# Optimization experiments

Hardware: AMD Instinct MI355X
Metric: run time of the kernel (lower is better)

Reference implementation:

```python
import jax, jax.numpy as jnp
import numpy as np

N_TYPES = 4
D_DESC = 256
H = 256
N_ATOMS = 131072


def setup_inputs() -> dict:
    key = jax.random.key(0)
    ks = jax.random.split(key, 8)
    descriptors = jax.random.normal(ks[0], (N_ATOMS, D_DESC), dtype=jnp.float32)
    elems = jax.random.randint(ks[1], (N_ATOMS,), 0, N_TYPES, dtype=jnp.int32)
    # Per-type MLP params: stacked over the type axis T.
    s1 = 1.0 / np.sqrt(D_DESC)
    s2 = 1.0 / np.sqrt(H)
    W1 = jax.random.normal(ks[2], (N_TYPES, D_DESC, H), dtype=jnp.float32) * s1
    b1 = jnp.zeros((N_TYPES, H), dtype=jnp.float32)
    W2 = jax.random.normal(ks[3], (N_TYPES, H, H), dtype=jnp.float32) * s2
    b2 = jnp.zeros((N_TYPES, H), dtype=jnp.float32)
    W3 = jax.random.normal(ks[4], (N_TYPES, H), dtype=jnp.float32) * s2  # output dim 1, squeezed
    b3 = jnp.zeros((N_TYPES,), dtype=jnp.float32)
    return {"descriptors": descriptors, "elems": elems,
            "W1": W1, "b1": b1, "W2": W2, "b2": b2, "W3": W3, "b3": b3}


def reference(descriptors, elems, W1, b1, W2, b2, W3, b3):
    # Equivalent to: for each atom, run the MLP subnet of its element type and
    # scatter the scalar output back to the per-atom attribute vector.
    # Vectorized as batched-per-type GEMMs followed by a per-atom type gather
    # (dense dispatch: fixed shapes, jit-friendly).
    # h1: [T, N, H]
    h1 = jnp.tanh(jnp.einsum('nd,tdh->tnh', descriptors, W1) + b1[:, None, :])
    h2 = jnp.tanh(jnp.einsum('tnh,thk->tnk', h1, W2) + b2[:, None, :])
    out_t = jnp.einsum('tnh,th->tn', h2, W3) + b3[:, None]  # [T, N]
    # select per-atom row according to its element type
    per_atom = out_t[elems, jnp.arange(out_t.shape[1])]  # [N]
    return per_atom
```

## Files before the change

### kernel.cpp

```cpp
#include <hip/hip_runtime.h>
#include <stdint.h>


typedef __attribute__((ext_vector_type(8))) short short8;
typedef __attribute__((ext_vector_type(4))) float f32x4;

#define NPB 256
#define NTY 4

__device__ __forceinline__ unsigned short f2bf(float f) {
    union { float f; uint32_t u; } v; v.f = f;
    uint32_t u = v.u;
    uint32_t r = (u + 0x7FFFu + ((u >> 16) & 1u)) >> 16;
    return (unsigned short)r;
}
__device__ __forceinline__ float fast_tanh(float x) {
    x = fminf(fmaxf(x, -10.0f), 10.0f);
    float e = __expf(2.0f * x);
    return (e - 1.0f) * __builtin_amdgcn_rcpf(e + 1.0f);
}


__global__ void count_k(const int* __restrict__ elems, int n, int chunk,
                        int* __restrict__ counts) {
    __shared__ int h[NTY];
    if (threadIdx.x < NTY) h[threadIdx.x] = 0;
    __syncthreads();
    const int start = blockIdx.x * chunk;
    const int end   = min(start + chunk, n);
    for (int i = start + threadIdx.x; i < end; i += blockDim.x)
        atomicAdd(&h[elems[i]], 1);
    __syncthreads();
    if (threadIdx.x < NTY) counts[threadIdx.x * NPB + blockIdx.x] = h[threadIdx.x];
}

__global__ void prefix_k(const int* __restrict__ counts,
                         int* __restrict__ cursor, int* __restrict__ hdr) {
    __shared__ int tot[NTY];
    const int t = threadIdx.x;
    if (t < NTY) {
        int s = 0;
        for (int b = 0; b < NPB; ++b) s += counts[t * NPB + b];
        tot[t] = s;
    }
    __syncthreads();
    if (t == 0) {
        int b = 0, tb = 0;
        for (int ty = 0; ty < NTY; ++ty) {
            hdr[ty]      = tot[ty];
            hdr[8 + ty]  = b;
            hdr[12 + ty] = tb;
            b  += tot[ty];
            tb += (tot[ty] + 63) >> 6;
        }
        hdr[16] = tb;
    }
    __syncthreads();
    if (t < NTY) {
        int run = hdr[8 + t];
        for (int b = 0; b < NPB; ++b) {
            cursor[t * NPB + b] = run;
            run += counts[t * NPB + b];
        }
    }
}

__global__ void scatter_k(const int* __restrict__ elems, int n, int chunk,
                          const int* __restrict__ cursor, int* __restrict__ sorted) {
    __shared__ int cur[NTY];
    if (threadIdx.x < NTY) cur[threadIdx.x] = cursor[threadIdx.x * NPB + blockIdx.x];
    __syncthreads();
    const int start = blockIdx.x * chunk;
    const int end   = min(start + chunk, n);
    for (int i = start + threadIdx.x; i < end; i += blockDim.x) {
        int ty  = elems[i];
        int pos = atomicAdd(&cur[ty], 1);
        sorted[pos] = i;
    }
}

__global__ void wconv_k(const float* __restrict__ W1, const float* __restrict__ W2,
                        unsigned short* __restrict__ w1s, unsigned short* __restrict__ w2s) {
    int gid  = blockIdx.x * blockDim.x + threadIdx.x;
    int lane = gid & 63;
    int ks   = (gid >> 6) & 7;
    int tile = (gid >> 9) & 15;
    int t    = (gid >> 13) & 3;
    int layer = gid >> 15;
    const float* W = layer ? W2 : W1;
    unsigned short* o = layer ? w2s : w1s;
    int dbase = ks * 32 + ((lane >> 4) << 3);
    int col   = tile * 16 + (lane & 15);
    unsigned short v[8];
#pragma unroll
    for (int j = 0; j < 8; ++j)
        v[j] = f2bf(W[(size_t)t * 65536 + (size_t)(dbase + j) * 256 + col]);
    unsigned short* dst = o + ((size_t)(t * 16 + tile) * 8 + ks) * 512 + lane * 8;
    *(short8*)dst = *(short8*)v;
}

__global__ __launch_bounds__(256, 4) void mlp_k(
    const float* __restrict__ desc,
    const float* __restrict__ b1g,
    const float* __restrict__ b2g,
    const float* __restrict__ W3,
    const float* __restrict__ b3,
    const int* __restrict__ hdr,
    const int* __restrict__ sorted,
    const unsigned short* __restrict__ w1s,
    const unsigned short* __restrict__ w2s,
    float* __restrict__ out)
{
    __shared__ __align__(16) char buf[32768];
    __shared__ float biasLds[512];
    __shared__ float part[4][64];

    const int tid  = threadIdx.x;
    const int lane = tid & 63;
    const int w    = tid >> 6;

    const int total = hdr[16];
    const int b = blockIdx.x;
    if (b >= total) return;

    int t = 3;
    if      (b < hdr[13]) t = 0;
    else if (b < hdr[14]) t = 1;
    else if (b < hdr[15]) t = 2;
    const int tloc   = b - hdr[12 + t];
    const int cnt    = hdr[t];
    const int base   = hdr[8 + t];
    const int astart = tloc * 64;

    biasLds[tid]       = b1g[t * 256 + tid];
    biasLds[256 + tid] = b2g[t * 256 + tid];

    {
        const int slot = tid >> 2;
        const int q    = tid & 3;
        const int g    = astart + slot;
        const int idx  = (g < cnt) ? sorted[base + g] : -1;
        const float4* row = (const float4*)(desc + (size_t)(idx < 0 ? 0 : idx) * 256);
#pragma unroll
        for (int i = 0; i < 16; ++i) {
            const int f = q + i * 4;
            float4 v;
            if (idx >= 0) v = row[f];
            else          v = make_float4(0.f, 0.f, 0.f, 0.f);
            unsigned short h4[4];
            h4[0] = f2bf(v.x); h4[1] = f2bf(v.y);
            h4[2] = f2bf(v.z); h4[3] = f2bf(v.w);
            const int off = slot * 512 + ((f * 8) ^ ((slot & 7) << 4));
            *(ushort4*)(buf + off) = *(ushort4*)h4;
        }
    }
    __syncthreads();

    const unsigned short* w1t = w1s + (size_t)t * (16 * 8 * 512);
    const unsigned short* w2t = w2s + (size_t)t * (16 * 8 * 512);

    f32x4 acc[4][4];
#pragma unroll
    for (int q = 0; q < 4; ++q)
#pragma unroll
        for (int nt = 0; nt < 4; ++nt)
            acc[q][nt] = (f32x4){0.f, 0.f, 0.f, 0.f};

#pragma unroll
    for (int ks = 0; ks < 8; ++ks) {
        short8 af[4];
#pragma unroll
        for (int q = 0; q < 4; ++q)
            af[q] = *(const short8*)(w1t + ((size_t)((w * 4 + q) * 8 + ks)) * 512 + lane * 8);
        short8 bh[4];
        const int colb = ks * 64 + ((lane >> 4) << 4);
#pragma unroll
        for (int nt = 0; nt < 4; ++nt) {
            const int row = nt * 16 + (lane & 15);
            const int off = row * 512 + (colb ^ ((row & 7) << 4));
            bh[nt] = *(const short8*)(buf + off);
        }
#pragma unroll
        for (int q = 0; q < 4; ++q)
#pragma unroll
            for (int nt = 0; nt < 4; ++nt)
                acc[q][nt] = __builtin_amdgcn_mfma_f32_16x16x32_bf16(af[q], bh[nt], acc[q][nt], 0, 0, 0);
    }
    __syncthreads();

    {
#pragma unroll
        for (int q = 0; q < 4; ++q) {
            const int h0 = (w * 4 + q) * 16 + ((lane >> 4) << 2);
#pragma unroll
            for (int nt = 0; nt < 4; ++nt) {
                const int atom = nt * 16 + (lane & 15);
                unsigned short h4[4];
#pragma unroll
                for (int r = 0; r < 4; ++r)
                    h4[r] = f2bf(fast_tanh(acc[q][nt][r] + biasLds[h0 + r]));
                const int off = atom * 512 + ((h0 * 2) ^ ((atom & 7) << 4));
                *(ushort4*)(buf + off) = *(ushort4*)h4;
            }
        }
    }
    __syncthreads();

    f32x4 acc2[4][4];
#pragma unroll
    for (int mt = 0; mt < 4; ++mt)
#pragma unroll
        for (int q = 0; q < 4; ++q)
            acc2[mt][q] = (f32x4){0.f, 0.f, 0.f, 0.f};

#pragma unroll
    for (int ks = 0; ks < 8; ++ks) {
        short8 bw[4];
#pragma unroll
        for (int q = 0; q < 4; ++q)
            bw[q] = *(const short8*)(w2t + ((size_t)((w * 4 + q) * 8 + ks)) * 512 + lane * 8);
        short8 ah[4];
        const int colb = ks * 64 + ((lane >> 4) << 4);
#pragma unroll
        for (int mt = 0; mt < 4; ++mt) {
            const int row = mt * 16 + (lane & 15);
            const int off = row * 512 + (colb ^ ((row & 7) << 4));
            ah[mt] = *(const short8*)(buf + off);
        }
#pragma unroll
        for (int mt = 0; mt < 4; ++mt)
#pragma unroll
            for (int q = 0; q < 4; ++q)
                acc2[mt][q] = __builtin_amdgcn_mfma_f32_16x16x32_bf16(ah[mt], bw[q], acc2[mt][q], 0, 0, 0);
    }

    float psum[4][4];
#pragma unroll
    for (int mt = 0; mt < 4; ++mt)
#pragma unroll
        for (int r = 0; r < 4; ++r)
            psum[mt][r] = 0.f;

#pragma unroll
    for (int q = 0; q < 4; ++q) {
        const int kout = (w * 4 + q) * 16 + (lane & 15);
        const float w3v = W3[t * 256 + kout];
        const float b2v = biasLds[256 + kout];
#pragma unroll
        for (int mt = 0; mt < 4; ++mt)
#pragma unroll
            for (int r = 0; r < 4; ++r)
                psum[mt][r] += fast_tanh(acc2[mt][q][r] + b2v) * w3v;
    }
#pragma unroll
    for (int m = 1; m <= 8; m <<= 1)
#pragma unroll
        for (int mt = 0; mt < 4; ++mt)
#pragma unroll
            for (int r = 0; r < 4; ++r)
                psum[mt][r] += __shfl_xor(psum[mt][r], m, 64);

    if ((lane & 15) == 0) {
        const int gq = lane >> 4;
#pragma unroll
        for (int mt = 0; mt < 4; ++mt)
#pragma unroll
            for (int r = 0; r < 4; ++r)
                part[w][mt * 16 + gq * 4 + r] = psum[mt][r];
    }
    __syncthreads();

    if (tid < 64) {
        const int gg = astart + tid;
        if (gg < cnt) {
            float v = part[0][tid] + part[1][tid] + part[2][tid] + part[3][tid] + b3[t];
            out[sorted[base + gg]] = v;
        }
    }
}

extern "C" void kernel_launch(void* const* d_in, const int* in_sizes, int n_in,
                              void* d_out, int out_size, void* d_ws, size_t ws_size,
                              hipStream_t stream) {
    const float* desc = (const float*)d_in[0];
    const int*   elems = (const int*)d_in[1];
    const float* W1 = (const float*)d_in[2];
    const float* b1 = (const float*)d_in[3];
    const float* W2 = (const float*)d_in[4];
    const float* b2 = (const float*)d_in[5];
    const float* W3 = (const float*)d_in[6];
    const float* b3 = (const float*)d_in[7];
    float* out = (float*)d_out;
    const int n = in_sizes[1];

    char* ws = (char*)d_ws;
    int* hdr    = (int*)ws;
    int* counts = (int*)(ws + 128);
    int* cursor = (int*)(ws + 128 + 4 * NPB * 4);
    int* sorted = (int*)(ws + 128 + 8 * NPB * 4);
    unsigned short* w1s = (unsigned short*)((char*)sorted + (size_t)n * 4);
    unsigned short* w2s = w1s + (size_t)4 * 16 * 8 * 512;

    const int chunk = (n + NPB - 1) / NPB;

    count_k<<<NPB, 256, 0, stream>>>(elems, n, chunk, counts);
    prefix_k<<<1, 64, 0, stream>>>(counts, cursor, hdr);
    scatter_k<<<NPB, 256, 0, stream>>>(elems, n, chunk, cursor, sorted);
    wconv_k<<<256, 256, 0, stream>>>(W1, W2, w1s, w2s);

    const int maxtiles = (n >> 6) + 4;
    mlp_k<<<maxtiles, 256, 0, stream>>>(desc, b1, b2, W3, b3,
                                        hdr, sorted, w1s, w2s, out);
}
```

Baseline: 117.4 us.

## Give each wave its own 16 atoms across all hidden units, removing block syncs

```diff
diff --git a/kernel.cpp b/kernel.cpp
--- a/kernel.cpp
+++ b/kernel.cpp
@@ -1,4 +1,5 @@
 #include <hip/hip_runtime.h>
+#include <hip/hip_bf16.h>
 #include <stdint.h>
 
 
@@ -111,13 +112,13 @@
     const unsigned short* __restrict__ w2s,
     float* __restrict__ out)
 {
-    __shared__ __align__(16) char buf[32768];
-    __shared__ float biasLds[512];
-    __shared__ float part[4][64];
+    __shared__ __align__(16) char h1lds[32768];
 
     const int tid  = threadIdx.x;
     const int lane = tid & 63;
     const int w    = tid >> 6;
+    const int a16  = lane & 15;
+    const int g    = lane >> 4;
 
     const int total = hdr[16];
     const int b = blockIdx.x;
@@ -132,149 +133,87 @@
     const int base   = hdr[8 + t];
     const int astart = tloc * 64;
 
-    biasLds[tid]       = b1g[t * 256 + tid];
-    biasLds[256 + tid] = b2g[t * 256 + tid];
-
-    {
-        const int slot = tid >> 2;
-        const int q    = tid & 3;
-        const int g    = astart + slot;
-        const int idx  = (g < cnt) ? sorted[base + g] : -1;
-        const float4* row = (const float4*)(desc + (size_t)(idx < 0 ? 0 : idx) * 256);
-#pragma unroll
-        for (int i = 0; i < 16; ++i) {
-            const int f = q + i * 4;
-            float4 v;
-            if (idx >= 0) v = row[f];
-            else          v = make_float4(0.f, 0.f, 0.f, 0.f);
-            unsigned short h4[4];
-            h4[0] = f2bf(v.x); h4[1] = f2bf(v.y);
-            h4[2] = f2bf(v.z); h4[3] = f2bf(v.w);
-            const int off = slot * 512 + ((f * 8) ^ ((slot & 7) << 4));
-            *(ushort4*)(buf + off) = *(ushort4*)h4;
-        }
-    }
-    __syncthreads();
+    const int am     = astart + w * 16 + a16;
+    const bool valid = (am < cnt);
+    const int idx    = valid ? sorted[base + am] : 0;
+    const float* xrow = desc + (size_t)idx * 256;
 
     const unsigned short* w1t = w1s + (size_t)t * (16 * 8 * 512);
     const unsigned short* w2t = w2s + (size_t)t * (16 * 8 * 512);
 
-    f32x4 acc[4][4];
-#pragma unroll
-    for (int q = 0; q < 4; ++q)
-#pragma unroll
-        for (int nt = 0; nt < 4; ++nt)
-            acc[q][nt] = (f32x4){0.f, 0.f, 0.f, 0.f};
+    f32x4 acc[16];
+#pragma unroll
+    for (int q = 0; q < 16; ++q) acc[q] = (f32x4){0.f, 0.f, 0.f, 0.f};
 
 #pragma unroll
     for (int ks = 0; ks < 8; ++ks) {
-        short8 af[4];
-#pragma unroll
-        for (int q = 0; q < 4; ++q)
-            af[q] = *(const short8*)(w1t + ((size_t)((w * 4 + q) * 8 + ks)) * 512 + lane * 8);
-        short8 bh[4];
-        const int colb = ks * 64 + ((lane >> 4) << 4);
-#pragma unroll
-        for (int nt = 0; nt < 4; ++nt) {
-            const int row = nt * 16 + (lane & 15);
-            const int off = row * 512 + (colb ^ ((row & 7) << 4));
-            bh[nt] = *(const short8*)(buf + off);
-        }
-#pragma unroll
-        for (int q = 0; q < 4; ++q)
-#pragma unroll
-            for (int nt = 0; nt < 4; ++nt)
-                acc[q][nt] = __builtin_amdgcn_mfma_f32_16x16x32_bf16(af[q], bh[nt], acc[q][nt], 0, 0, 0);
-    }
-    __syncthreads();
-
-    {
-#pragma unroll
-        for (int q = 0; q < 4; ++q) {
-            const int h0 = (w * 4 + q) * 16 + ((lane >> 4) << 2);
-#pragma unroll
-            for (int nt = 0; nt < 4; ++nt) {
-                const int atom = nt * 16 + (lane & 15);
-                unsigned short h4[4];
-#pragma unroll
-                for (int r = 0; r < 4; ++r)
-                    h4[r] = f2bf(fast_tanh(acc[q][nt][r] + biasLds[h0 + r]));
-                const int off = atom * 512 + ((h0 * 2) ^ ((atom & 7) << 4));
-                *(ushort4*)(buf + off) = *(ushort4*)h4;
-            }
-        }
-    }
-    __syncthreads();
-
-    f32x4 acc2[4][4];
-#pragma unroll
-    for (int mt = 0; mt < 4; ++mt)
-#pragma unroll
-        for (int q = 0; q < 4; ++q)
-            acc2[mt][q] = (f32x4){0.f, 0.f, 0.f, 0.f};
+        const float4 v0 = *(const float4*)(xrow + ks * 32 + g * 8);
+        const float4 v1 = *(const float4*)(xrow + ks * 32 + g * 8 + 4);
+        union { short8 s; __hip_bfloat162 h[4]; } bu;
+        bu.h[0] = __float22bfloat162_rn(make_float2(v0.x, v0.y));
+        bu.h[1] = __float22bfloat162_rn(make_float2(v0.z, v0.w));
+        bu.h[2] = __float22bfloat162_rn(make_float2(v1.x, v1.y));
+        bu.h[3] = __float22bfloat162_rn(make_float2(v1.z, v1.w));
+#pragma unroll
+        for (int q = 0; q < 16; ++q) {
+            const short8 af = *(const short8*)(w1t + ((size_t)(q * 8 + ks)) * 512 + lane * 8);
+            acc[q] = __builtin_amdgcn_mfma_f32_16x16x32_bf16(af, bu.s, acc[q], 0, 0, 0);
+        }
+    }
+
+    char* myh1 = h1lds + w * 8192;
+#pragma unroll
+    for (int q = 0; q < 16; ++q) {
+        const float4 bb = *(const float4*)(b1g + t * 256 + q * 16 + g * 4);
+        const float z0 = fast_tanh(acc[q][0] + bb.x);
+        const float z1 = fast_tanh(acc[q][1] + bb.y);
+        const float z2 = fast_tanh(acc[q][2] + bb.z);
+        const float z3 = fast_tanh(acc[q][3] + bb.w);
+        union { uint64_t u; __hip_bfloat162 h[2]; } hw;
+        hw.h[0] = __float22bfloat162_rn(make_float2(z0, z1));
+        hw.h[1] = __float22bfloat162_rn(make_float2(z2, z3));
+        const int off = a16 * 512 + ((q * 32 + g * 8) ^ ((a16 & 7) << 4));
+        *(uint64_t*)(myh1 + off) = hw.u;
+    }
+
+    f32x4 acc2[16];
+#pragma unroll
+    for (int q = 0; q < 16; ++q) acc2[q] = (f32x4){0.f, 0.f, 0.f, 0.f};
 
 #pragma unroll
     for (int ks = 0; ks < 8; ++ks) {
-        short8 bw[4];
-#pragma unroll
-        for (int q = 0; q < 4; ++q)
-            bw[q] = *(const short8*)(w2t + ((size_t)((w * 4 + q) * 8 + ks)) * 512 + lane * 8);
-        short8 ah[4];
-        const int colb = ks * 64 + ((lane >> 4) << 4);
-#pragma unroll
-        for (int mt = 0; mt < 4; ++mt) {
-            const int row = mt * 16 + (lane & 15);
-            const int off = row * 512 + (colb ^ ((row & 7) << 4));
-            ah[mt] = *(const short8*)(buf + off);
-        }
-#pragma unroll
-        for (int mt = 0; mt < 4; ++mt)
-#pragma unroll
-            for (int q = 0; q < 4; ++q)
-                acc2[mt][q] = __builtin_amdgcn_mfma_f32_16x16x32_bf16(ah[mt], bw[q], acc2[mt][q], 0, 0, 0);
-    }
-
-    float psum[4][4];
-#pragma unroll
-    for (int mt = 0; mt < 4; ++mt)
+        const int off = a16 * 512 + ((ks * 64 + g * 16) ^ ((a16 & 7) << 4));
+        const short8 ah = *(const short8*)(myh1 + off);
+#pragma unroll
+        for (int q = 0; q < 16; ++q) {
+            const short8 bw = *(const short8*)(w2t + ((size_t)(q * 8 + ks)) * 512 + lane * 8);
+            acc2[q] = __builtin_amdgcn_mfma_f32_16x16x32_bf16(ah, bw, acc2[q], 0, 0, 0);
+        }
+    }
+
+    float psum[4] = {0.f, 0.f, 0.f, 0.f};
+#pragma unroll
+    for (int q = 0; q < 16; ++q) {
+        const int kout = q * 16 + a16;
+        const float b2v = b2g[t * 256 + kout];
+        const float w3v = W3[t * 256 + kout];
 #pragma unroll
         for (int r = 0; r < 4; ++r)
-            psum[mt][r] = 0.f;
-
-#pragma unroll
-    for (int q = 0; q < 4; ++q) {
-        const int kout = (w * 4 + q) * 16 + (lane & 15);
-        const float w3v = W3[t * 256 + kout];
-        const float b2v = biasLds[256 + kout];
-#pragma unroll
-        for (int mt = 0; mt < 4; ++mt)
-#pragma unroll
-            for (int r = 0; r < 4; ++r)
-                psum[mt][r] += fast_tanh(acc2[mt][q][r] + b2v) * w3v;
+            psum[r] += fast_tanh(acc2[q][r] + b2v) * w3v;
     }
 #pragma unroll
     for (int m = 1; m <= 8; m <<= 1)
 #pragma unroll
-        for (int mt = 0; mt < 4; ++mt)
-#pragma unroll
-            for (int r = 0; r < 4; ++r)
-                psum[mt][r] += __shfl_xor(psum[mt][r], m, 64);
-
-    if ((lane & 15) == 0) {
-        const int gq = lane >> 4;
-#pragma unroll
-        for (int mt = 0; mt < 4; ++mt)
-#pragma unroll
-            for (int r = 0; r < 4; ++r)
-                part[w][mt * 16 + gq * 4 + r] = psum[mt][r];
-    }
-    __syncthreads();
-
-    if (tid < 64) {
-        const int gg = astart + tid;
-        if (gg < cnt) {
-            float v = part[0][tid] + part[1][tid] + part[2][tid] + part[3][tid] + b3[t];
-            out[sorted[base + gg]] = v;
+        for (int r = 0; r < 4; ++r)
+            psum[r] += __shfl_xor(psum[r], m, 64);
+
+    if (a16 == 0) {
+        const float b3v = b3[t];
+#pragma unroll
+        for (int r = 0; r < 4; ++r) {
+            const int am2 = astart + w * 16 + g * 4 + r;
+            if (am2 < cnt)
+                out[sorted[base + am2]] = psum[r] + b3v;
         }
     }
 }
```

New measurement: 228.3 us. +94.5%, slower.

## Make MLP kernel persistent with double-buffered prefetch of next tile's descriptors

Applied to the files above, without the earlier changes.

```diff
diff --git a/kernel.cpp b/kernel.cpp
--- a/kernel.cpp
+++ b/kernel.cpp
@@ -1,4 +1,5 @@
 #include <hip/hip_runtime.h>
+#include <hip/hip_bf16.h>
 #include <stdint.h>
 
 
@@ -7,6 +8,7 @@
 
 #define NPB 256
 #define NTY 4
+#define MLPGRID 512
 
 __device__ __forceinline__ unsigned short f2bf(float f) {
     union { float f; uint32_t u; } v; v.f = f;
@@ -99,7 +101,7 @@
     *(short8*)dst = *(short8*)v;
 }
 
-__global__ __launch_bounds__(256, 4) void mlp_k(
+__global__ __launch_bounds__(256, 2) void mlp_k(
     const float* __restrict__ desc,
     const float* __restrict__ b1g,
     const float* __restrict__ b2g,
@@ -111,172 +113,214 @@
     const unsigned short* __restrict__ w2s,
     float* __restrict__ out)
 {
-    __shared__ __align__(16) char buf[32768];
-    __shared__ float biasLds[512];
+    __shared__ __align__(16) char buf[2][32768];
     __shared__ float part[4][64];
 
     const int tid  = threadIdx.x;
     const int lane = tid & 63;
     const int w    = tid >> 6;
+    const int slot = tid >> 2;
+    const int q4   = tid & 3;
 
     const int total = hdr[16];
-    const int b = blockIdx.x;
-    if (b >= total) return;
-
-    int t = 3;
-    if      (b < hdr[13]) t = 0;
-    else if (b < hdr[14]) t = 1;
-    else if (b < hdr[15]) t = 2;
-    const int tloc   = b - hdr[12 + t];
-    const int cnt    = hdr[t];
-    const int base   = hdr[8 + t];
-    const int astart = tloc * 64;
-
-    biasLds[tid]       = b1g[t * 256 + tid];
-    biasLds[256 + tid] = b2g[t * 256 + tid];
+    int tile = blockIdx.x;
+    if (tile >= total) return;
+
+#define TILEINFO(TL, T, CNT, BASE, AST)                          \
+    {                                                            \
+        T = 3;                                                   \
+        if      ((TL) < hdr[13]) T = 0;                          \
+        else if ((TL) < hdr[14]) T = 1;                          \
+        else if ((TL) < hdr[15]) T = 2;                          \
+        CNT = hdr[T]; BASE = hdr[8 + T];                         \
+        AST = ((TL) - hdr[12 + T]) * 64;                         \
+    }
+
+    float4 xr[16];
 
     {
-        const int slot = tid >> 2;
-        const int q    = tid & 3;
-        const int g    = astart + slot;
-        const int idx  = (g < cnt) ? sorted[base + g] : -1;
-        const float4* row = (const float4*)(desc + (size_t)(idx < 0 ? 0 : idx) * 256);
+        int t0, cnt0, base0, as0;
+        TILEINFO(tile, t0, cnt0, base0, as0);
+        const int gg  = as0 + slot;
+        const int idx = (gg < cnt0) ? sorted[base0 + gg] : 0;
+        const float* row = desc + (size_t)idx * 256;
+#pragma unroll
+        for (int i = 0; i < 16; ++i)
+            xr[i] = *(const float4*)(row + (q4 + i * 4) * 4);
 #pragma unroll
         for (int i = 0; i < 16; ++i) {
-            const int f = q + i * 4;
-            float4 v;
-            if (idx >= 0) v = row[f];
-            else          v = make_float4(0.f, 0.f, 0.f, 0.f);
+            const int f = q4 + i * 4;
             unsigned short h4[4];
-            h4[0] = f2bf(v.x); h4[1] = f2bf(v.y);
-            h4[2] = f2bf(v.z); h4[3] = f2bf(v.w);
+            h4[0] = f2bf(xr[i].x); h4[1] = f2bf(xr[i].y);
+            h4[2] = f2bf(xr[i].z); h4[3] = f2bf(xr[i].w);
             const int off = slot * 512 + ((f * 8) ^ ((slot & 7) << 4));
-            *(ushort4*)(buf + off) = *(ushort4*)h4;
-        }
-    }
-    __syncthreads();
-
-    const unsigned short* w1t = w1s + (size_t)t * (16 * 8 * 512);
-    const unsigned short* w2t = w2s + (size_t)t * (16 * 8 * 512);
-
-    f32x4 acc[4][4];
-#pragma unroll
-    for (int q = 0; q < 4; ++q)
-#pragma unroll
-        for (int nt = 0; nt < 4; ++nt)
-            acc[q][nt] = (f32x4){0.f, 0.f, 0.f, 0.f};
-
-#pragma unroll
-    for (int ks = 0; ks < 8; ++ks) {
-        short8 af[4];
+            *(ushort4*)(buf[0] + off) = *(ushort4*)h4;
+        }
+    }
+    __syncthreads();
+
+    for (int k = 0;; ++k) {
+        const int cur = k & 1;
+        const int nxt = tile + MLPGRID;
+        const bool has_next = (nxt < total);
+
+        if (has_next) {
+            int tn, cntn, basen, asn;
+            TILEINFO(nxt, tn, cntn, basen, asn);
+            const int gg  = asn + slot;
+            const int idx = (gg < cntn) ? sorted[basen + gg] : 0;
+            const float* row = desc + (size_t)idx * 256;
+#pragma unroll
+            for (int i = 0; i < 16; ++i)
+                xr[i] = *(const float4*)(row + (q4 + i * 4) * 4);
+        }
+
+        int t, cnt, base, astart;
+        TILEINFO(tile, t, cnt, base, astart);
+        const unsigned short* w1t = w1s + (size_t)t * (16 * 8 * 512);
+        const unsigned short* w2t = w2s + (size_t)t * (16 * 8 * 512);
+        const char* cb = buf[cur];
+
+        f32x4 acc[4][4];
 #pragma unroll
         for (int q = 0; q < 4; ++q)
-            af[q] = *(const short8*)(w1t + ((size_t)((w * 4 + q) * 8 + ks)) * 512 + lane * 8);
-        short8 bh[4];
-        const int colb = ks * 64 + ((lane >> 4) << 4);
-#pragma unroll
-        for (int nt = 0; nt < 4; ++nt) {
-            const int row = nt * 16 + (lane & 15);
-            const int off = row * 512 + (colb ^ ((row & 7) << 4));
-            bh[nt] = *(const short8*)(buf + off);
-        }
-#pragma unroll
-        for (int q = 0; q < 4; ++q)
 #pragma unroll
             for (int nt = 0; nt < 4; ++nt)
-                acc[q][nt] = __builtin_amdgcn_mfma_f32_16x16x32_bf16(af[q], bh[nt], acc[q][nt], 0, 0, 0);
-    }
-    __syncthreads();
-
-    {
+                acc[q][nt] = (f32x4){0.f, 0.f, 0.f, 0.f};
+
+#pragma unroll
+        for (int ks = 0; ks < 8; ++ks) {
+            short8 af[4];
+#pragma unroll
+            for (int q = 0; q < 4; ++q)
+                af[q] = *(const short8*)(w1t + ((size_t)((w * 4 + q) * 8 + ks)) * 512 + lane * 8);
+            short8 bh[4];
+            const int colb = ks * 64 + ((lane >> 4) << 4);
+#pragma unroll
+            for (int nt = 0; nt < 4; ++nt) {
+                const int row = nt * 16 + (lane & 15);
+                const int off = row * 512 + (colb ^ ((row & 7) << 4));
+                bh[nt] = *(const short8*)(cb + off);
+            }
+#pragma unroll
+            for (int q = 0; q < 4; ++q)
+#pragma unroll
+                for (int nt = 0; nt < 4; ++nt)
+                    acc[q][nt] = __builtin_amdgcn_mfma_f32_16x16x32_bf16(af[q], bh[nt], acc[q][nt], 0, 0, 0);
+        }
+        __syncthreads();
+
+        {
+            char* hb = buf[cur];
+#pragma unroll
+            for (int q = 0; q < 4; ++q) {
+                const int h0 = (w * 4 + q) * 16 + ((lane >> 4) << 2);
+                const float4 bb = *(const float4*)(b1g + t * 256 + h0);
+#pragma unroll
+                for (int nt = 0; nt < 4; ++nt) {
+                    const int atom = nt * 16 + (lane & 15);
+                    unsigned short h4[4];
+                    h4[0] = f2bf(fast_tanh(acc[q][nt][0] + bb.x));
+                    h4[1] = f2bf(fast_tanh(acc[q][nt][1] + bb.y));
+                    h4[2] = f2bf(fast_tanh(acc[q][nt][2] + bb.z));
+                    h4[3] = f2bf(fast_tanh(acc[q][nt][3] + bb.w));
+                    const int off = atom * 512 + ((h0 * 2) ^ ((atom & 7) << 4));
+                    *(ushort4*)(hb + off) = *(ushort4*)h4;
+                }
+            }
+        }
+        __syncthreads();
+
+        f32x4 acc2[4][4];
+#pragma unroll
+        for (int mt = 0; mt < 4; ++mt)
+#pragma unroll
+            for (int q = 0; q < 4; ++q)
+                acc2[mt][q] = (f32x4){0.f, 0.f, 0.f, 0.f};
+
+#pragma unroll
+        for (int ks = 0; ks < 8; ++ks) {
+            short8 bw[4];
+#pragma unroll
+            for (int q = 0; q < 4; ++q)
+                bw[q] = *(const short8*)(w2t + ((size_t)((w * 4 + q) * 8 + ks)) * 512 + lane * 8);
+            short8 ah[4];
+            const int colb = ks * 64 + ((lane >> 4) << 4);
+#pragma unroll
+            for (int mt = 0; mt < 4; ++mt) {
+                const int row = mt * 16 + (lane & 15);
+                const int off = row * 512 + (colb ^ ((row & 7) << 4));
+                ah[mt] = *(const short8*)(cb + off);
+            }
+#pragma unroll
+            for (int mt = 0; mt < 4; ++mt)
+#pragma unroll
+                for (int q = 0; q < 4; ++q)
+                    acc2[mt][q] = __builtin_amdgcn_mfma_f32_16x16x32_bf16(ah[mt], bw[q], acc2[mt][q], 0, 0, 0);
+        }
+
+        float psum[4][4];
+#pragma unroll
+        for (int mt = 0; mt < 4; ++mt)
+#pragma unroll
+            for (int r = 0; r < 4; ++r)
+                psum[mt][r] = 0.f;
+
 #pragma unroll
         for (int q = 0; q < 4; ++q) {
-            const int h0 = (w * 4 + q) * 16 + ((lane >> 4) << 2);
-#pragma unroll
-            for (int nt = 0; nt < 4; ++nt) {
-                const int atom = nt * 16 + (lane & 15);
+            const int kout = (w * 4 + q) * 16 + (lane & 15);
+            const float w3v = W3[t * 256 + kout];
+            const float b2v = b2g[t * 256 + kout];
+#pragma unroll
+            for (int mt = 0; mt < 4; ++mt)
+#pragma unroll
+                for (int r = 0; r < 4; ++r)
+                    psum[mt][r] += fast_tanh(acc2[mt][q][r] + b2v) * w3v;
+        }
+#pragma unroll
+        for (int m = 1; m <= 8; m <<= 1)
+#pragma unroll
+            for (int mt = 0; mt < 4; ++mt)
+#pragma unroll
+                for (int r = 0; r < 4; ++r)
+                    psum[mt][r] += __shfl_xor(psum[mt][r], m, 64);
+
+        if ((lane & 15) == 0) {
+            const int gq = lane >> 4;
+#pragma unroll
+            for (int mt = 0; mt < 4; ++mt)
+#pragma unroll
+                for (int r = 0; r < 4; ++r)
+                    part[w][mt * 16 + gq * 4 + r] = psum[mt][r];
+        }
+        __syncthreads();
+
+        if (tid < 64) {
+            const int gg = astart + tid;
+            if (gg < cnt) {
+                float v = part[0][tid] + part[1][tid] + part[2][tid] + part[3][tid] + b3[t];
+                out[sorted[base + gg]] = v;
+            }
+        }
+
+        if (has_next) {
+            char* nb = buf[cur ^ 1];
+#pragma unroll
+            for (int i = 0; i < 16; ++i) {
+                const int f = q4 + i * 4;
                 unsigned short h4[4];
-#pragma unroll
-                for (int r = 0; r < 4; ++r)
-                    h4[r] = f2bf(fast_tanh(acc[q][nt][r] + biasLds[h0 + r]));
-                const int off = atom * 512 + ((h0 * 2) ^ ((atom & 7) << 4));
-                *(ushort4*)(buf + off) = *(ushort4*)h4;
-            }
-        }
-    }
-    __syncthreads();
-
-    f32x4 acc2[4][4];
-#pragma unroll
-    for (int mt = 0; mt < 4; ++mt)
-#pragma unroll
-        for (int q = 0; q < 4; ++q)
-            acc2[mt][q] = (f32x4){0.f, 0.f, 0.f, 0.f};
-
-#pragma unroll
-    for (int ks = 0; ks < 8; ++ks) {
-        short8 bw[4];
-#pragma unroll
-        for (int q = 0; q < 4; ++q)
-            bw[q] = *(const short8*)(w2t + ((size_t)((w * 4 + q) * 8 + ks)) * 512 + lane * 8);
-        short8 ah[4];
-        const int colb = ks * 64 + ((lane >> 4) << 4);
-#pragma unroll
-        for (int mt = 0; mt < 4; ++mt) {
-            const int row = mt * 16 + (lane & 15);
-            const int off = row * 512 + (colb ^ ((row & 7) << 4));
-            ah[mt] = *(const short8*)(buf + off);
-        }
-#pragma unroll
-        for (int mt = 0; mt < 4; ++mt)
-#pragma unroll
-            for (int q = 0; q < 4; ++q)
-                acc2[mt][q] = __builtin_amdgcn_mfma_f32_16x16x32_bf16(ah[mt], bw[q], acc2[mt][q], 0, 0, 0);
-    }
-
-    float psum[4][4];
-#pragma unroll
-    for (int mt = 0; mt < 4; ++mt)
-#pragma unroll
-        for (int r = 0; r < 4; ++r)
-            psum[mt][r] = 0.f;
-
-#pragma unroll
-    for (int q = 0; q < 4; ++q) {
-        const int kout = (w * 4 + q) * 16 + (lane & 15);
-        const float w3v = W3[t * 256 + kout];
-        const float b2v = biasLds[256 + kout];
-#pragma unroll
-        for (int mt = 0; mt < 4; ++mt)
-#pragma unroll
-            for (int r = 0; r < 4; ++r)
-                psum[mt][r] += fast_tanh(acc2[mt][q][r] + b2v) * w3v;
-    }
-#pragma unroll
-    for (int m = 1; m <= 8; m <<= 1)
-#pragma unroll
-        for (int mt = 0; mt < 4; ++mt)
-#pragma unroll
-            for (int r = 0; r < 4; ++r)
-                psum[mt][r] += __shfl_xor(psum[mt][r], m, 64);
-
-    if ((lane & 15) == 0) {
-        const int gq = lane >> 4;
-#pragma unroll
-        for (int mt = 0; mt < 4; ++mt)
-#pragma unroll
-            for (int r = 0; r < 4; ++r)
-                part[w][mt * 16 + gq * 4 + r] = psum[mt][r];
-    }
-    __syncthreads();
-
-    if (tid < 64) {
-        const int gg = astart + tid;
-        if (gg < cnt) {
-            float v = part[0][tid] + part[1][tid] + part[2][tid] + part[3][tid] + b3[t];
-            out[sorted[base + gg]] = v;
-        }
-    }
+                h4[0] = f2bf(xr[i].x); h4[1] = f2bf(xr[i].y);
+                h4[2] = f2bf(xr[i].z); h4[3] = f2bf(xr[i].w);
+                const int off = slot * 512 + ((f * 8) ^ ((slot & 7) << 4));
+                *(ushort4*)(nb + off) = *(ushort4*)h4;
+            }
+        }
+        __syncthreads();
+
+        if (!has_next) break;
+        tile = nxt;
+    }
+#undef TILEINFO
 }
 
 extern "C" void kernel_launch(void* const* d_in, const int* in_sizes, int n_in,
@@ -308,7 +352,6 @@
     scatter_k<<<NPB, 256, 0, stream>>>(elems, n, chunk, cursor, sorted);
     wconv_k<<<256, 256, 0, stream>>>(W1, W2, w1s, w2s);
 
-    const int maxtiles = (n >> 6) + 4;
-    mlp_k<<<maxtiles, 256, 0, stream>>>(desc, b1, b2, W3, b3,
-                                        hdr, sorted, w1s, w2s, out);
-}
+    mlp_k<<<MLPGRID, 256, 0, stream>>>(desc, b1, b2, W3, b3,
+                                       hdr, sorted, w1s, w2s, out);
+}
```

Result: slower. 179.9 us (+53.3%).

## Split fused MLP kernel into two layer kernels with bf16 h1 in global memory

Applied to the files above, without the earlier changes.

```diff
diff --git a/kernel.cpp b/kernel.cpp
--- a/kernel.cpp
+++ b/kernel.cpp
@@ -1,4 +1,5 @@
 #include <hip/hip_runtime.h>
+#include <hip/hip_bf16.h>
 #include <stdint.h>
 
 
@@ -7,6 +8,9 @@
 
 #define NPB 256
 #define NTY 4
+
+typedef __attribute__((address_space(3))) void lds_void;
+typedef __attribute__((address_space(1))) const void glb_void;
 
 __device__ __forceinline__ unsigned short f2bf(float f) {
     union { float f; uint32_t u; } v; v.f = f;
@@ -99,112 +103,153 @@
     *(short8*)dst = *(short8*)v;
 }
 
-__global__ __launch_bounds__(256, 4) void mlp_k(
+#define TILEINFO(TL, T, CNT, BASE, AST)                          \
+    {                                                            \
+        T = 3;                                                   \
+        if      ((TL) < hdr[13]) T = 0;                          \
+        else if ((TL) < hdr[14]) T = 1;                          \
+        else if ((TL) < hdr[15]) T = 2;                          \
+        CNT = hdr[T]; BASE = hdr[8 + T];                         \
+        AST = ((TL) - hdr[12 + T]) * 64;                         \
+    }
+
+__global__ __launch_bounds__(256, 2) void mlp1_k(
     const float* __restrict__ desc,
     const float* __restrict__ b1g,
+    const int* __restrict__ hdr,
+    const int* __restrict__ sorted,
+    const unsigned short* __restrict__ w1s,
+    unsigned short* __restrict__ h1g)
+{
+    __shared__ __align__(16) char buf[32768];
+
+    const int tid  = threadIdx.x;
+    const int lane = tid & 63;
+    const int w    = tid >> 6;
+
+    const int b = blockIdx.x;
+    if (b >= hdr[16]) return;
+    int t, cnt, base, astart;
+    TILEINFO(b, t, cnt, base, astart);
+
+    {
+        const int slot = tid >> 2;
+        const int q4   = tid & 3;
+        const int gg   = astart + slot;
+        const int idx  = (gg < cnt) ? sorted[base + gg] : 0;
+        const float4* row = (const float4*)(desc + (size_t)idx * 256);
+#pragma unroll
+        for (int i = 0; i < 16; ++i) {
+            const int f = q4 + i * 4;
+            const float4 v = row[f];
+            unsigned short h4[4];
+            h4[0] = f2bf(v.x); h4[1] = f2bf(v.y);
+            h4[2] = f2bf(v.z); h4[3] = f2bf(v.w);
+            const int off = slot * 512 + ((f * 8) ^ ((slot & 7) << 4));
+            *(ushort4*)(buf + off) = *(ushort4*)h4;
+        }
+    }
+    __syncthreads();
+
+    const unsigned short* w1t = w1s + (size_t)t * (16 * 8 * 512);
+
+    f32x4 acc[4][4];
+#pragma unroll
+    for (int q = 0; q < 4; ++q)
+#pragma unroll
+        for (int nt = 0; nt < 4; ++nt)
+            acc[q][nt] = (f32x4){0.f, 0.f, 0.f, 0.f};
+
+#pragma unroll
+    for (int ks = 0; ks < 8; ++ks) {
+        short8 af[4];
+#pragma unroll
+        for (int q = 0; q < 4; ++q)
+            af[q] = *(const short8*)(w1t + ((size_t)((w * 4 + q) * 8 + ks)) * 512 + lane * 8);
+        short8 bh[4];
+        const int colb = ks * 64 + ((lane >> 4) << 4);
+#pragma unroll
+        for (int nt = 0; nt < 4; ++nt) {
+            const int row = nt * 16 + (lane & 15);
+            const int off = row * 512 + (colb ^ ((row & 7) << 4));
+            bh[nt] = *(const short8*)(buf + off);
+        }
+#pragma unroll
+        for (int q = 0; q < 4; ++q)
+#pragma unroll
+            for (int nt = 0; nt < 4; ++nt)
+                acc[q][nt] = __builtin_amdgcn_mfma_f32_16x16x32_bf16(af[q], bh[nt], acc[q][nt], 0, 0, 0);
+    }
+    __syncthreads();
+
+#pragma unroll
+    for (int q = 0; q < 4; ++q) {
+        const int h0 = (w * 4 + q) * 16 + ((lane >> 4) << 2);
+        const float4 bb = *(const float4*)(b1g + t * 256 + h0);
+#pragma unroll
+        for (int nt = 0; nt < 4; ++nt) {
+            const int atom = nt * 16 + (lane & 15);
+            unsigned short h4[4];
+            h4[0] = f2bf(fast_tanh(acc[q][nt][0] + bb.x));
+            h4[1] = f2bf(fast_tanh(acc[q][nt][1] + bb.y));
+            h4[2] = f2bf(fast_tanh(acc[q][nt][2] + bb.z));
+            h4[3] = f2bf(fast_tanh(acc[q][nt][3] + bb.w));
+            const int off = atom * 512 + ((h0 * 2) ^ ((atom & 7) << 4));
+            *(ushort4*)(buf + off) = *(ushort4*)h4;
+        }
+    }
+    __syncthreads();
+
+    {
+        const int p  = tid & 31;
+        const int a0 = tid >> 5;
+#pragma unroll
+        for (int i = 0; i < 8; ++i) {
+            const int atom = a0 + i * 8;
+            const int gg   = astart + atom;
+            const uint4 v = *(const uint4*)(buf + atom * 512 + ((p * 16) ^ ((atom & 7) << 4)));
+            if (gg < cnt)
+                *(uint4*)((char*)h1g + (size_t)(base + gg) * 512 + p * 16) = v;
+        }
+    }
+}
+
+__global__ __launch_bounds__(256, 2) void mlp2_k(
     const float* __restrict__ b2g,
     const float* __restrict__ W3,
     const float* __restrict__ b3,
     const int* __restrict__ hdr,
     const int* __restrict__ sorted,
-    const unsigned short* __restrict__ w1s,
     const unsigned short* __restrict__ w2s,
+    const unsigned short* __restrict__ h1g,
     float* __restrict__ out)
 {
     __shared__ __align__(16) char buf[32768];
-    __shared__ float biasLds[512];
     __shared__ float part[4][64];
 
     const int tid  = threadIdx.x;
     const int lane = tid & 63;
     const int w    = tid >> 6;
 
-    const int total = hdr[16];
     const int b = blockIdx.x;
-    if (b >= total) return;
-
-    int t = 3;
-    if      (b < hdr[13]) t = 0;
-    else if (b < hdr[14]) t = 1;
-    else if (b < hdr[15]) t = 2;
-    const int tloc   = b - hdr[12 + t];
-    const int cnt    = hdr[t];
-    const int base   = hdr[8 + t];
-    const int astart = tloc * 64;
-
-    biasLds[tid]       = b1g[t * 256 + tid];
-    biasLds[256 + tid] = b2g[t * 256 + tid];
-
-    {
-        const int slot = tid >> 2;
-        const int q    = tid & 3;
-        const int g    = astart + slot;
-        const int idx  = (g < cnt) ? sorted[base + g] : -1;
-        const float4* row = (const float4*)(desc + (size_t)(idx < 0 ? 0 : idx) * 256);
-#pragma unroll
-        for (int i = 0; i < 16; ++i) {
-            const int f = q + i * 4;
-            float4 v;
-            if (idx >= 0) v = row[f];
-            else          v = make_float4(0.f, 0.f, 0.f, 0.f);
-            unsigned short h4[4];
-            h4[0] = f2bf(v.x); h4[1] = f2bf(v.y);
-            h4[2] = f2bf(v.z); h4[3] = f2bf(v.w);
-            const int off = slot * 512 + ((f * 8) ^ ((slot & 7) << 4));
-            *(ushort4*)(buf + off) = *(ushort4*)h4;
-        }
-    }
-    __syncthreads();
-
-    const unsigned short* w1t = w1s + (size_t)t * (16 * 8 * 512);
+    if (b >= hdr[16]) return;
+    int t, cnt, base, astart;
+    TILEINFO(b, t, cnt, base, astart);
+
+#pragma unroll
+    for (int i = 0; i < 8; ++i) {
+        const int row = w * 16 + i * 2 + (lane >> 5);
+        const int p   = lane & 31;
+        const int gg  = astart + row;
+        const size_t srow = (size_t)(base + ((gg < cnt) ? gg : 0));
+        const char* src = (const char*)h1g + srow * 512 + ((p * 16) ^ ((row & 7) << 4));
+        char* dst = buf + w * 8192 + i * 1024;
+        __builtin_amdgcn_global_load_lds((glb_void*)src, (lds_void*)dst, 16, 0, 0);
+    }
+    asm volatile("s_waitcnt vmcnt(0)" ::: "memory");
+    __syncthreads();
+
     const unsigned short* w2t = w2s + (size_t)t * (16 * 8 * 512);
-
-    f32x4 acc[4][4];
-#pragma unroll
-    for (int q = 0; q < 4; ++q)
-#pragma unroll
-        for (int nt = 0; nt < 4; ++nt)
-            acc[q][nt] = (f32x4){0.f, 0.f, 0.f, 0.f};
-
-#pragma unroll
-    for (int ks = 0; ks < 8; ++ks) {
-        short8 af[4];
-#pragma unroll
-        for (int q = 0; q < 4; ++q)
-            af[q] = *(const short8*)(w1t + ((size_t)((w * 4 + q) * 8 + ks)) * 512 + lane * 8);
-        short8 bh[4];
-        const int colb = ks * 64 + ((lane >> 4) << 4);
-#pragma unroll
-        for (int nt = 0; nt < 4; ++nt) {
-            const int row = nt * 16 + (lane & 15);
-            const int off = row * 512 + (colb ^ ((row & 7) << 4));
-            bh[nt] = *(const short8*)(buf + off);
-        }
-#pragma unroll
-        for (int q = 0; q < 4; ++q)
-#pragma unroll
-            for (int nt = 0; nt < 4; ++nt)
-                acc[q][nt] = __builtin_amdgcn_mfma_f32_16x16x32_bf16(af[q], bh[nt], acc[q][nt], 0, 0, 0);
-    }
-    __syncthreads();
-
-    {
-#pragma unroll
-        for (int q = 0; q < 4; ++q) {
-            const int h0 = (w * 4 + q) * 16 + ((lane >> 4) << 2);
-#pragma unroll
-            for (int nt = 0; nt < 4; ++nt) {
-                const int atom = nt * 16 + (lane & 15);
-                unsigned short h4[4];
-#pragma unroll
-                for (int r = 0; r < 4; ++r)
-                    h4[r] = f2bf(fast_tanh(acc[q][nt][r] + biasLds[h0 + r]));
-                const int off = atom * 512 + ((h0 * 2) ^ ((atom & 7) << 4));
-                *(ushort4*)(buf + off) = *(ushort4*)h4;
-            }
-        }
-    }
-    __syncthreads();
 
     f32x4 acc2[4][4];
 #pragma unroll
@@ -245,7 +290,7 @@
     for (int q = 0; q < 4; ++q) {
         const int kout = (w * 4 + q) * 16 + (lane & 15);
         const float w3v = W3[t * 256 + kout];
-        const float b2v = biasLds[256 + kout];
+        const float b2v = b2g[t * 256 + kout];
 #pragma unroll
         for (int mt = 0; mt < 4; ++mt)
 #pragma unroll
@@ -300,6 +345,7 @@
     int* sorted = (int*)(ws + 128 + 8 * NPB * 4);
     unsigned short* w1s = (unsigned short*)((char*)sorted + (size_t)n * 4);
     unsigned short* w2s = w1s + (size_t)4 * 16 * 8 * 512;
+    unsigned short* h1g = w2s + (size_t)4 * 16 * 8 * 512;
 
     const int chunk = (n + NPB - 1) / NPB;
 
@@ -309,6 +355,6 @@
     wconv_k<<<256, 256, 0, stream>>>(W1, W2, w1s, w2s);
 
     const int maxtiles = (n >> 6) + 4;
-    mlp_k<<<maxtiles, 256, 0, stream>>>(desc, b1, b2, W3, b3,
-                                        hdr, sorted, w1s, w2s, out);
-}
+    mlp1_k<<<maxtiles, 256, 0, stream>>>(desc, b1, hdr, sorted, w1s, h1g);
+    mlp2_k<<<maxtiles, 256, 0, stream>>>(b2, W3, b3, hdr, sorted, w2s, h1g, out);
+}
```

Measured after the change: 107.0 us, median of 3. -8.9%, faster.
